# Kernel optimization log

Hardware: AMD Instinct MI355X
Metric: run time of the kernel (lower is better)

Reference implementation:

```python
import jax, jax.numpy as jnp
import numpy as np

N_NODES = 100000
N_EDGES = 1000000
EMB_DIM = 64
N_LAYERS = 5
NUM_CLASS = 10
NUM_GRAPHS = 128
BN_EPS = 1e-5


def setup_inputs() -> dict:
    key = jax.random.key(0)
    ks = jax.random.split(key, 16)
    s = 0.05
    inp = {
        "x": jnp.zeros((N_NODES,), dtype=jnp.int64),
        "edge_index": jax.random.randint(ks[0], (2, N_EDGES), 0, N_NODES, dtype=jnp.int64),
        "edge_attr": jax.random.normal(ks[1], (N_EDGES, 7), dtype=jnp.float32),
        "batch": jnp.sort(jax.random.randint(ks[2], (N_NODES,), 0, NUM_GRAPHS, dtype=jnp.int64)),
        # parameters
        "node_table": jax.random.normal(ks[3], (1, EMB_DIM), dtype=jnp.float32) * s,
        "ew": jax.random.normal(ks[4], (N_LAYERS, 7, EMB_DIM), dtype=jnp.float32) * s,   # edge_encoder weight
        "eb": jax.random.normal(ks[5], (N_LAYERS, EMB_DIM), dtype=jnp.float32) * s,
        "w1": jax.random.normal(ks[6], (N_LAYERS, EMB_DIM, EMB_DIM), dtype=jnp.float32) * s,
        "b1": jax.random.normal(ks[7], (N_LAYERS, EMB_DIM), dtype=jnp.float32) * s,
        "w2": jax.random.normal(ks[8], (N_LAYERS, EMB_DIM, EMB_DIM), dtype=jnp.float32) * s,
        "b2": jax.random.normal(ks[9], (N_LAYERS, EMB_DIM), dtype=jnp.float32) * s,
        "gamma": jnp.ones((N_LAYERS, EMB_DIM), dtype=jnp.float32),
        "beta": jnp.zeros((N_LAYERS, EMB_DIM), dtype=jnp.float32),
        "pw": jax.random.normal(ks[10], (EMB_DIM, NUM_CLASS), dtype=jnp.float32) * s,
        "pb": jnp.zeros((NUM_CLASS,), dtype=jnp.float32),
    }
    return inp


def reference(x, edge_index, edge_attr, batch, node_table, ew, eb, w1, b1, w2, b2, gamma, beta, pw, pb):
    n = x.shape[0]
    src, dst = edge_index[0], edge_index[1]
    h = node_table[x]  # [N, D] node embedding lookup (all index 0)
    for l in range(N_LAYERS):
        edge_emb = edge_attr @ ew[l] + eb[l]                      # [E, D]
        msg = jax.nn.relu(h[src] + edge_emb)                      # gather + add + relu
        agg = jax.ops.segment_sum(msg, dst, num_segments=n)       # scatter-add
        z = h + agg                                               # (1 + eps)*x with eps=0
        z = jax.nn.relu(z @ w1[l] + b1[l]) @ w2[l] + b2[l]        # GIN MLP
        mu = z.mean(axis=0)
        var = z.var(axis=0)                                       # biased var, matches BN training
        z = (z - mu) * jax.lax.rsqrt(var + BN_EPS) * gamma[l] + beta[l]
        if l != N_LAYERS - 1:
            z = jax.nn.relu(z)                                    # dropout is identity (eval)
        h = z
    # global mean pool over graphs
    sums = jax.ops.segment_sum(h, batch, num_segments=NUM_GRAPHS)           # [B, D]
    cnt = jax.ops.segment_sum(jnp.ones((n,), h.dtype), batch, num_segments=NUM_GRAPHS)
    h_graph = sums / jnp.maximum(cnt, 1.0)[:, None]
    return h_graph @ pw + pb
```

## Files before the change

### kernel.cpp

```cpp
#include <hip/hip_runtime.h>


__global__ void hist_k(const int* __restrict__ dst, int* __restrict__ cnt, int E) {
  int stride = gridDim.x * blockDim.x;
  for (int i = blockIdx.x * blockDim.x + threadIdx.x; i < E; i += stride)
    atomicAdd(&cnt[dst[i]], 1);
}

__global__ void scan_a_k(const int* __restrict__ deg, int* __restrict__ rowptr,
                         int* __restrict__ bsum, int n) {
  __shared__ int s[256];
  int i = blockIdx.x * 256 + threadIdx.x;
  int v = (i < n) ? deg[i] : 0;
  s[threadIdx.x] = v;
  __syncthreads();
  for (int off = 1; off < 256; off <<= 1) {
    int t = (threadIdx.x >= off) ? s[threadIdx.x - off] : 0;
    __syncthreads();
    s[threadIdx.x] += t;
    __syncthreads();
  }
  if (i < n) rowptr[i] = s[threadIdx.x] - v;
  if (threadIdx.x == 255) bsum[blockIdx.x] = s[255];
}

__global__ void scan_b_k(int* __restrict__ bsum, int nb) {
  __shared__ int s[512];
  int t = threadIdx.x;
  int v = (t < nb) ? bsum[t] : 0;
  s[t] = v;
  __syncthreads();
  for (int off = 1; off < 512; off <<= 1) {
    int u = (t >= off) ? s[t - off] : 0;
    __syncthreads();
    s[t] += u;
    __syncthreads();
  }
  if (t < nb) bsum[t] = s[t] - v;
}

__global__ void scan_c_k(int* __restrict__ rowptr, int* __restrict__ cur,
                         const int* __restrict__ bsum, int n, int E) {
  int i = blockIdx.x * 256 + threadIdx.x;
  if (i < n) {
    int r = rowptr[i] + bsum[blockIdx.x];
    rowptr[i] = r;
    cur[i] = r;
  }
  if (i == 0) rowptr[n] = E;
}

__global__ void scatter_k(const int* __restrict__ src, const int* __restrict__ dst,
                          int* __restrict__ cur, float* __restrict__ sea,
                          const float* __restrict__ ea, int E) {
  int stride = gridDim.x * blockDim.x;
  for (int i = blockIdx.x * blockDim.x + threadIdx.x; i < E; i += stride) {
    int d = dst[i];
    int pos = atomicAdd(&cur[d], 1);
    float* o = sea + (size_t)pos * 8;
    const float* a = ea + (size_t)i * 7;
#pragma unroll
    for (int k = 0; k < 7; k++) o[k] = a[k];
    o[7] = __int_as_float(src[i]);
  }
}

template<bool FIRST>
__global__ void agg_k(const float* __restrict__ hprev, const int* __restrict__ x,
                      const float* __restrict__ ntab, const int* __restrict__ rowptr,
                      const float* __restrict__ sea, const float* __restrict__ ew,
                      const float* __restrict__ eb, const float* __restrict__ scsh,
                      float* __restrict__ zout, int n, int layer) {
  int wid = (blockIdx.x * blockDim.x + threadIdx.x) >> 6;
  if (wid >= n) return;
  int lane = threadIdx.x & 63;
  const float* ewl = ew + layer * 448;
  float ew_[7];
#pragma unroll
  for (int k = 0; k < 7; k++) ew_[k] = ewl[k * 64 + lane];
  float ebv = eb[layer * 64 + lane];
  float sc = 1.f, sh = 0.f;
  if (!FIRST) { sc = scsh[lane]; sh = scsh[64 + lane]; }

  auto H = [&](int row) -> float {
    if (FIRST) {
      return ntab[x[row] * 64 + lane];
    } else {
      float v = hprev[(size_t)row * 64 + lane];
      return fmaxf(fmaf(v, sc, sh), 0.f);
    }
  };

  float acc = H(wid);
  int p0 = __builtin_amdgcn_readfirstlane(rowptr[wid]);
  int p1 = __builtin_amdgcn_readfirstlane(rowptr[wid + 1]);
  for (int p = p0; p < p1; p += 8) {
    const float* R[8];
    int srcv[8];
#pragma unroll
    for (int u = 0; u < 8; u++) {
      int t = p + u;
      int q = t < p1 ? t : p1 - 1;
      R[u] = sea + (size_t)q * 8;
      srcv[u] = __builtin_amdgcn_readfirstlane(__float_as_int(R[u][7]));
    }
    float h[8];
#pragma unroll
    for (int u = 0; u < 8; u++) h[u] = H(srcv[u]);
    float m[8];
#pragma unroll
    for (int u = 0; u < 8; u++) m[u] = ebv;
#pragma unroll
    for (int k = 0; k < 7; k++) {
#pragma unroll
      for (int u = 0; u < 8; u++) m[u] = fmaf(R[u][k], ew_[k], m[u]);
    }
#pragma unroll
    for (int u = 0; u < 8; u++) {
      float contrib = fmaxf(h[u] + m[u], 0.f);
      acc += (p + u < p1) ? contrib : 0.f;
    }
  }
  zout[(size_t)wid * 64 + lane] = acc;
}

__global__ __launch_bounds__(256, 3)
void mlp_k(const float* __restrict__ zin, const float* __restrict__ w1g,
           const float* __restrict__ b1, const float* __restrict__ w2g,
           const float* __restrict__ b2, float* __restrict__ zout,
           float* __restrict__ bnstats, int n, int layer) {
  __shared__ float As[64 * 129];
  __shared__ float Ws[64 * 64];
  __shared__ float red[128];
  int tid = threadIdx.x;
  int tx = tid & 15, ty = tid >> 4;
  if (tid < 128) red[tid] = 0.f;
  int r0 = blockIdx.x * 128;

  {
    const float4* gz = (const float4*)(zin + (size_t)r0 * 64);
#pragma unroll
    for (int it = 0; it < 8; it++) {
      int f4 = it * 256 + tid;
      int row = f4 >> 4, kq = f4 & 15;
      float4 v = make_float4(0.f, 0.f, 0.f, 0.f);
      if (r0 + row < n) v = gz[f4];
      As[(4 * kq + 0) * 129 + row] = v.x;
      As[(4 * kq + 1) * 129 + row] = v.y;
      As[(4 * kq + 2) * 129 + row] = v.z;
      As[(4 * kq + 3) * 129 + row] = v.w;
    }
    const float* wa = w1g + layer * 4096;
#pragma unroll
    for (int it = 0; it < 16; it++) Ws[it * 256 + tid] = wa[it * 256 + tid];
  }
  __syncthreads();

  const float4 b1v = *(const float4*)(b1 + layer * 64 + tx * 4);
  float t[8][4];
#pragma unroll
  for (int rr = 0; rr < 8; rr++) {
    t[rr][0] = b1v.x; t[rr][1] = b1v.y; t[rr][2] = b1v.z; t[rr][3] = b1v.w;
  }
#pragma unroll 4
  for (int k = 0; k < 64; k++) {
    float a[8];
#pragma unroll
    for (int rr = 0; rr < 8; rr++) a[rr] = As[k * 129 + ty * 8 + rr];
    float4 b = *(const float4*)&Ws[k * 64 + tx * 4];
#pragma unroll
    for (int rr = 0; rr < 8; rr++) {
      t[rr][0] = fmaf(a[rr], b.x, t[rr][0]);
      t[rr][1] = fmaf(a[rr], b.y, t[rr][1]);
      t[rr][2] = fmaf(a[rr], b.z, t[rr][2]);
      t[rr][3] = fmaf(a[rr], b.w, t[rr][3]);
    }
  }
  __syncthreads();

#pragma unroll
  for (int cc = 0; cc < 4; cc++)
#pragma unroll
    for (int rr = 0; rr < 8; rr++)
      As[(tx * 4 + cc) * 129 + ty * 8 + rr] = fmaxf(t[rr][cc], 0.f);
  {
    const float* wb = w2g + layer * 4096;
#pragma unroll
    for (int it = 0; it < 16; it++) Ws[it * 256 + tid] = wb[it * 256 + tid];
  }
  __syncthreads();

  const float4 b2v = *(const float4*)(b2 + layer * 64 + tx * 4);
  float o[8][4];
#pragma unroll
  for (int rr = 0; rr < 8; rr++) {
    o[rr][0] = b2v.x; o[rr][1] = b2v.y; o[rr][2] = b2v.z; o[rr][3] = b2v.w;
  }
#pragma unroll 4
  for (int k = 0; k < 64; k++) {
    float a[8];
#pragma unroll
    for (int rr = 0; rr < 8; rr++) a[rr] = As[k * 129 + ty * 8 + rr];
    float4 b = *(const float4*)&Ws[k * 64 + tx * 4];
#pragma unroll
    for (int rr = 0; rr < 8; rr++) {
      o[rr][0] = fmaf(a[rr], b.x, o[rr][0]);
      o[rr][1] = fmaf(a[rr], b.y, o[rr][1]);
      o[rr][2] = fmaf(a[rr], b.z, o[rr][2]);
      o[rr][3] = fmaf(a[rr], b.w, o[rr][3]);
    }
  }

  float s1[4] = {0.f, 0.f, 0.f, 0.f}, s2[4] = {0.f, 0.f, 0.f, 0.f};
#pragma unroll
  for (int rr = 0; rr < 8; rr++) {
    int grow = r0 + ty * 8 + rr;
    if (grow < n) {
      float4 v = make_float4(o[rr][0], o[rr][1], o[rr][2], o[rr][3]);
      *(float4*)(zout + (size_t)grow * 64 + tx * 4) = v;
#pragma unroll
      for (int cc = 0; cc < 4; cc++) {
        s1[cc] += o[rr][cc];
        s2[cc] = fmaf(o[rr][cc], o[rr][cc], s2[cc]);
      }
    }
  }
#pragma unroll
  for (int cc = 0; cc < 4; cc++) {
    s1[cc] += __shfl_xor(s1[cc], 16); s1[cc] += __shfl_xor(s1[cc], 32);
    s2[cc] += __shfl_xor(s2[cc], 16); s2[cc] += __shfl_xor(s2[cc], 32);
  }
  if ((tid & 48) == 0) {
#pragma unroll
    for (int cc = 0; cc < 4; cc++) {
      atomicAdd(&red[tx * 4 + cc], s1[cc]);
      atomicAdd(&red[64 + tx * 4 + cc], s2[cc]);
    }
  }
  __syncthreads();
  if (tid < 128) atomicAdd(&bnstats[tid], red[tid]);
}

__global__ void fin_k(float* __restrict__ bnstats, const float* __restrict__ gamma,
                      const float* __restrict__ beta, float* __restrict__ scsh,
                      int n, int layer) {
  int d = threadIdx.x;
  float mu = bnstats[d] / (float)n;
  float var = bnstats[64 + d] / (float)n - mu * mu;
  float sc = gamma[layer * 64 + d] * rsqrtf(var + 1e-5f);
  scsh[d] = sc;
  scsh[64 + d] = beta[layer * 64 + d] - mu * sc;
  bnstats[d] = 0.f;
  bnstats[64 + d] = 0.f;
}

__global__ void pool_k(const float* __restrict__ z2, const float* __restrict__ scsh,
                       const int* __restrict__ batch, float* __restrict__ gsum,
                       float* __restrict__ gcnt, int n, int ch) {
  int wid = (blockIdx.x * blockDim.x + threadIdx.x) >> 6;
  int lane = threadIdx.x & 63;
  int v0 = wid * ch;
  if (v0 >= n) return;
  int v1 = v0 + ch; if (v1 > n) v1 = n;
  float sc = scsh[lane], sh = scsh[64 + lane];
  int curb = batch[v0];
  float acc = 0.f;
  int cnt = 0;
  for (int v = v0; v < v1; v++) {
    int b = batch[v];
    if (b != curb) {
      atomicAdd(&gsum[curb * 64 + lane], acc);
      if (lane == 0) atomicAdd(&gcnt[curb], (float)cnt);
      acc = 0.f; cnt = 0; curb = b;
    }
    acc += fmaf(z2[(size_t)v * 64 + lane], sc, sh);
    cnt++;
  }
  atomicAdd(&gsum[curb * 64 + lane], acc);
  if (lane == 0) atomicAdd(&gcnt[curb], (float)cnt);
}

__global__ void head_k(const float* __restrict__ gsum, const float* __restrict__ gcnt,
                       const float* __restrict__ pw, const float* __restrict__ pb,
                       float* __restrict__ out, int B, int C) {
  for (int idx = threadIdx.x; idx < B * C; idx += blockDim.x) {
    int g = idx / C, c = idx % C;
    float inv = 1.f / fmaxf(gcnt[g], 1.f);
    float s = pb[c];
    for (int d = 0; d < 64; d++)
      s = fmaf(gsum[g * 64 + d] * inv, pw[d * C + c], s);
    out[idx] = s;
  }
}

extern "C" void kernel_launch(void* const* d_in, const int* in_sizes, int n_in,
                              void* d_out, int out_size, void* d_ws, size_t ws_size,
                              hipStream_t stream) {
  const int*   x     = (const int*)d_in[0];
  const int*   ei    = (const int*)d_in[1];
  const float* ea    = (const float*)d_in[2];
  const int*   batch = (const int*)d_in[3];
  const float* ntab  = (const float*)d_in[4];
  const float* ew    = (const float*)d_in[5];
  const float* eb    = (const float*)d_in[6];
  const float* w1    = (const float*)d_in[7];
  const float* b1    = (const float*)d_in[8];
  const float* w2    = (const float*)d_in[9];
  const float* b2    = (const float*)d_in[10];
  const float* gamma = (const float*)d_in[11];
  const float* beta  = (const float*)d_in[12];
  const float* pw    = (const float*)d_in[13];
  const float* pb    = (const float*)d_in[14];
  float* out = (float*)d_out;

  int N = in_sizes[0];
  int E = in_sizes[1] / 2;
  int L = in_sizes[6] / 64;
  int C = in_sizes[14];
  int B = out_size / C;

  const int* src = ei;
  const int* dst = ei + E;

  char* ws = (char*)d_ws;
  auto alloc = [&](size_t bytes) -> char* {
    char* p = ws;
    ws += (bytes + 255) & ~(size_t)255;
    return p;
  };
  float* zA      = (float*)alloc((size_t)N * 64 * 4);
  float* zB      = (float*)alloc((size_t)N * 64 * 4);
  int*   rowptr  = (int*)alloc((size_t)(N + 1) * 4);
  int*   cur     = (int*)alloc((size_t)N * 4);
  float* sea     = (float*)alloc((size_t)E * 8 * 4);
  int*   bsum    = (int*)alloc(512 * 4);
  float* bnstats = (float*)alloc(128 * 4);
  float* scsh    = (float*)alloc(128 * 4);
  float* gsum    = (float*)alloc((size_t)B * 64 * 4);
  float* gcnt    = (float*)alloc((size_t)B * 4);

  hipMemsetAsync(cur, 0, (size_t)N * 4, stream);
  hipMemsetAsync(bnstats, 0, 128 * 4, stream);
  hipMemsetAsync(gsum, 0, (size_t)B * 64 * 4, stream);
  hipMemsetAsync(gcnt, 0, (size_t)B * 4, stream);

  hist_k<<<1024, 256, 0, stream>>>(dst, cur, E);
  int NB = (N + 255) / 256;
  scan_a_k<<<NB, 256, 0, stream>>>(cur, rowptr, bsum, N);
  scan_b_k<<<1, 512, 0, stream>>>(bsum, NB);
  scan_c_k<<<NB, 256, 0, stream>>>(rowptr, cur, bsum, N, E);
  scatter_k<<<1024, 256, 0, stream>>>(src, dst, cur, sea, ea, E);

  int aggBlocks = (N * 64 + 255) / 256;
  int mlpBlocks = (N + 127) / 128;
  for (int l = 0; l < L; l++) {
    if (l == 0)
      agg_k<true><<<aggBlocks, 256, 0, stream>>>(zB, x, ntab, rowptr, sea,
                                                 ew, eb, scsh, zA, N, l);
    else
      agg_k<false><<<aggBlocks, 256, 0, stream>>>(zB, x, ntab, rowptr, sea,
                                                  ew, eb, scsh, zA, N, l);
    mlp_k<<<mlpBlocks, 256, 0, stream>>>(zA, w1, b1, w2, b2, zB, bnstats, N, l);
    fin_k<<<1, 64, 0, stream>>>(bnstats, gamma, beta, scsh, N, l);
  }

  int ch = 128;
  int poolWaves = (N + ch - 1) / ch;
  int poolBlocks = (poolWaves + 3) / 4;
  pool_k<<<poolBlocks, 256, 0, stream>>>(zB, scsh, batch, gsum, gcnt, N, ch);
  head_k<<<1, 256, 0, stream>>>(gsum, gcnt, pw, pb, out, B, C);
}
```

Baseline: 716.6 us.

## Fuse BN finalize into consumers, multi-node agg waves, vectorize MLP and scatter

Removes the per-layer fin_k launch by giving each layer its own stats slot and computing BN scale and shift inside the next agg kernel and inside pool_k. The agg kernel now processes 8 nodes per wave with a 4-edge unrolled loop, and adds a constant-table mode for a single-row node table that skips the neighbor gather entirely in layer 0. It also widens scatter stores and MLP shared-memory reads to float4 (stride 132), changes launch sizes, and adds unroll hints. Processing several nodes per wave reduces wave count but cuts parallelism and may worsen load imbalance.

After: 654.1 us. 1.1x faster.

```diff
diff --git a/kernel.cpp b/kernel.cpp
--- a/kernel.cpp
+++ b/kernel.cpp
@@ -57,80 +57,115 @@
   for (int i = blockIdx.x * blockDim.x + threadIdx.x; i < E; i += stride) {
     int d = dst[i];
     int pos = atomicAdd(&cur[d], 1);
-    float* o = sea + (size_t)pos * 8;
     const float* a = ea + (size_t)i * 7;
-#pragma unroll
-    for (int k = 0; k < 7; k++) o[k] = a[k];
-    o[7] = __int_as_float(src[i]);
-  }
-}
-
-template<bool FIRST>
-__global__ void agg_k(const float* __restrict__ hprev, const int* __restrict__ x,
-                      const float* __restrict__ ntab, const int* __restrict__ rowptr,
-                      const float* __restrict__ sea, const float* __restrict__ ew,
-                      const float* __restrict__ eb, const float* __restrict__ scsh,
-                      float* __restrict__ zout, int n, int layer) {
-  int wid = (blockIdx.x * blockDim.x + threadIdx.x) >> 6;
-  if (wid >= n) return;
+    float4 lo = make_float4(a[0], a[1], a[2], a[3]);
+    float4 hi = make_float4(a[4], a[5], a[6], __int_as_float(src[i]));
+    float4* o = (float4*)(sea + (size_t)pos * 8);
+    o[0] = lo;
+    o[1] = hi;
+  }
+}
+
+#define NPW 8
+template<int MODE>
+__global__ __launch_bounds__(256)
+void agg_k(const float* __restrict__ hprev, const int* __restrict__ x,
+           const float* __restrict__ ntab, const int* __restrict__ rowptr,
+           const float* __restrict__ sea, const float* __restrict__ ewl,
+           const float* __restrict__ ebl, const float* __restrict__ stats,
+           const float* __restrict__ gam, const float* __restrict__ bet,
+           float* __restrict__ zout, int n) {
+  int wv = (blockIdx.x * blockDim.x + threadIdx.x) >> 6;
   int lane = threadIdx.x & 63;
-  const float* ewl = ew + layer * 448;
+  int g0 = wv * NPW;
+  if (g0 >= n) return;
+  int gend = g0 + NPW; if (gend > n) gend = n;
+
   float ew_[7];
 #pragma unroll
   for (int k = 0; k < 7; k++) ew_[k] = ewl[k * 64 + lane];
-  float ebv = eb[layer * 64 + lane];
-  float sc = 1.f, sh = 0.f;
-  if (!FIRST) { sc = scsh[lane]; sh = scsh[64 + lane]; }
-
-  auto H = [&](int row) -> float {
-    if (FIRST) {
-      return ntab[x[row] * 64 + lane];
+  float ebv = ebl[lane];
+
+  float cnst = 0.f, sc = 1.f, sh = 0.f;
+  if (MODE == 0) cnst = ntab[lane];
+  if (MODE == 2) {
+    float s1 = stats[lane], s2 = stats[64 + lane];
+    float mu = s1 / (float)n;
+    float var = s2 / (float)n - mu * mu;
+    sc = gam[lane] * rsqrtf(var + 1e-5f);
+    sh = bet[lane] - mu * sc;
+  }
+
+  auto Hg = [&](int row) -> float {
+    if (MODE == 1) {
+      int xv = __builtin_amdgcn_readfirstlane(x[row]);
+      return ntab[(size_t)xv * 64 + lane];
     } else {
       float v = hprev[(size_t)row * 64 + lane];
       return fmaxf(fmaf(v, sc, sh), 0.f);
     }
   };
 
-  float acc = H(wid);
-  int p0 = __builtin_amdgcn_readfirstlane(rowptr[wid]);
-  int p1 = __builtin_amdgcn_readfirstlane(rowptr[wid + 1]);
-  for (int p = p0; p < p1; p += 8) {
-    const float* R[8];
-    int srcv[8];
-#pragma unroll
-    for (int u = 0; u < 8; u++) {
-      int t = p + u;
-      int q = t < p1 ? t : p1 - 1;
-      R[u] = sea + (size_t)q * 8;
-      srcv[u] = __builtin_amdgcn_readfirstlane(__float_as_int(R[u][7]));
-    }
-    float h[8];
-#pragma unroll
-    for (int u = 0; u < 8; u++) h[u] = H(srcv[u]);
-    float m[8];
-#pragma unroll
-    for (int u = 0; u < 8; u++) m[u] = ebv;
-#pragma unroll
-    for (int k = 0; k < 7; k++) {
-#pragma unroll
-      for (int u = 0; u < 8; u++) m[u] = fmaf(R[u][k], ew_[k], m[u]);
-    }
-#pragma unroll
-    for (int u = 0; u < 8; u++) {
-      float contrib = fmaxf(h[u] + m[u], 0.f);
-      acc += (p + u < p1) ? contrib : 0.f;
-    }
-  }
-  zout[(size_t)wid * 64 + lane] = acc;
-}
-
+  int pcur = __builtin_amdgcn_readfirstlane(rowptr[g0]);
+  for (int nd = g0; nd < gend; nd++) {
+    int pnext = __builtin_amdgcn_readfirstlane(rowptr[nd + 1]);
+    float acc;
+    if (MODE == 0) acc = cnst;
+    else acc = Hg(nd);
+    int p = pcur;
+    for (; p + 4 <= pnext; p += 4) {
+      const float* R0 = sea + (size_t)p * 8;
+      const float* R1 = R0 + 8;
+      const float* R2 = R0 + 16;
+      const float* R3 = R0 + 24;
+      float h0 = 0.f, h1 = 0.f, h2 = 0.f, h3 = 0.f;
+      if (MODE != 0) {
+        int s0 = __builtin_amdgcn_readfirstlane(__float_as_int(R0[7]));
+        int s1 = __builtin_amdgcn_readfirstlane(__float_as_int(R1[7]));
+        int s2 = __builtin_amdgcn_readfirstlane(__float_as_int(R2[7]));
+        int s3 = __builtin_amdgcn_readfirstlane(__float_as_int(R3[7]));
+        h0 = Hg(s0); h1 = Hg(s1); h2 = Hg(s2); h3 = Hg(s3);
+      } else {
+        h0 = h1 = h2 = h3 = cnst;
+      }
+      float m0 = ebv, m1 = ebv, m2 = ebv, m3 = ebv;
+#pragma unroll
+      for (int k = 0; k < 7; k++) {
+        m0 = fmaf(R0[k], ew_[k], m0);
+        m1 = fmaf(R1[k], ew_[k], m1);
+        m2 = fmaf(R2[k], ew_[k], m2);
+        m3 = fmaf(R3[k], ew_[k], m3);
+      }
+      acc += fmaxf(h0 + m0, 0.f);
+      acc += fmaxf(h1 + m1, 0.f);
+      acc += fmaxf(h2 + m2, 0.f);
+      acc += fmaxf(h3 + m3, 0.f);
+    }
+    for (; p < pnext; p++) {
+      const float* R0 = sea + (size_t)p * 8;
+      float h0 = cnst;
+      if (MODE != 0) {
+        int s0 = __builtin_amdgcn_readfirstlane(__float_as_int(R0[7]));
+        h0 = Hg(s0);
+      }
+      float m0 = ebv;
+#pragma unroll
+      for (int k = 0; k < 7; k++) m0 = fmaf(R0[k], ew_[k], m0);
+      acc += fmaxf(h0 + m0, 0.f);
+    }
+    zout[(size_t)nd * 64 + lane] = acc;
+    pcur = pnext;
+  }
+}
+
+#define ASTR 132
 __global__ __launch_bounds__(256, 3)
-void mlp_k(const float* __restrict__ zin, const float* __restrict__ w1g,
-           const float* __restrict__ b1, const float* __restrict__ w2g,
-           const float* __restrict__ b2, float* __restrict__ zout,
-           float* __restrict__ bnstats, int n, int layer) {
-  __shared__ float As[64 * 129];
-  __shared__ float Ws[64 * 64];
+void mlp_k(const float* __restrict__ zin, const float* __restrict__ w1l,
+           const float* __restrict__ b1l, const float* __restrict__ w2l,
+           const float* __restrict__ b2l, float* __restrict__ zout,
+           float* __restrict__ statslot, int n) {
+  __shared__ float As[64 * ASTR];
+  __shared__ float Ws[4096];
   __shared__ float red[128];
   int tid = threadIdx.x;
   int tx = tid & 15, ty = tid >> 4;
@@ -145,29 +180,30 @@
       int row = f4 >> 4, kq = f4 & 15;
       float4 v = make_float4(0.f, 0.f, 0.f, 0.f);
       if (r0 + row < n) v = gz[f4];
-      As[(4 * kq + 0) * 129 + row] = v.x;
-      As[(4 * kq + 1) * 129 + row] = v.y;
-      As[(4 * kq + 2) * 129 + row] = v.z;
-      As[(4 * kq + 3) * 129 + row] = v.w;
-    }
-    const float* wa = w1g + layer * 4096;
-#pragma unroll
-    for (int it = 0; it < 16; it++) Ws[it * 256 + tid] = wa[it * 256 + tid];
-  }
-  __syncthreads();
-
-  const float4 b1v = *(const float4*)(b1 + layer * 64 + tx * 4);
+      As[(4 * kq + 0) * ASTR + row] = v.x;
+      As[(4 * kq + 1) * ASTR + row] = v.y;
+      As[(4 * kq + 2) * ASTR + row] = v.z;
+      As[(4 * kq + 3) * ASTR + row] = v.w;
+    }
+    const float4* wa = (const float4*)w1l;
+    float4* wd = (float4*)Ws;
+#pragma unroll
+    for (int it = 0; it < 4; it++) wd[it * 256 + tid] = wa[it * 256 + tid];
+  }
+  __syncthreads();
+
+  const float4 b1v = *(const float4*)(b1l + tx * 4);
   float t[8][4];
 #pragma unroll
   for (int rr = 0; rr < 8; rr++) {
     t[rr][0] = b1v.x; t[rr][1] = b1v.y; t[rr][2] = b1v.z; t[rr][3] = b1v.w;
   }
-#pragma unroll 4
+#pragma unroll 8
   for (int k = 0; k < 64; k++) {
-    float a[8];
-#pragma unroll
-    for (int rr = 0; rr < 8; rr++) a[rr] = As[k * 129 + ty * 8 + rr];
+    float4 aA = *(const float4*)&As[k * ASTR + ty * 8];
+    float4 aB = *(const float4*)&As[k * ASTR + ty * 8 + 4];
     float4 b = *(const float4*)&Ws[k * 64 + tx * 4];
+    float a[8] = {aA.x, aA.y, aA.z, aA.w, aB.x, aB.y, aB.z, aB.w};
 #pragma unroll
     for (int rr = 0; rr < 8; rr++) {
       t[rr][0] = fmaf(a[rr], b.x, t[rr][0]);
@@ -182,26 +218,27 @@
   for (int cc = 0; cc < 4; cc++)
 #pragma unroll
     for (int rr = 0; rr < 8; rr++)
-      As[(tx * 4 + cc) * 129 + ty * 8 + rr] = fmaxf(t[rr][cc], 0.f);
+      As[(tx * 4 + cc) * ASTR + ty * 8 + rr] = fmaxf(t[rr][cc], 0.f);
   {
-    const float* wb = w2g + layer * 4096;
-#pragma unroll
-    for (int it = 0; it < 16; it++) Ws[it * 256 + tid] = wb[it * 256 + tid];
-  }
-  __syncthreads();
-
-  const float4 b2v = *(const float4*)(b2 + layer * 64 + tx * 4);
+    const float4* wb = (const float4*)w2l;
+    float4* wd = (float4*)Ws;
+#pragma unroll
+    for (int it = 0; it < 4; it++) wd[it * 256 + tid] = wb[it * 256 + tid];
+  }
+  __syncthreads();
+
+  const float4 b2v = *(const float4*)(b2l + tx * 4);
   float o[8][4];
 #pragma unroll
   for (int rr = 0; rr < 8; rr++) {
     o[rr][0] = b2v.x; o[rr][1] = b2v.y; o[rr][2] = b2v.z; o[rr][3] = b2v.w;
   }
-#pragma unroll 4
+#pragma unroll 8
   for (int k = 0; k < 64; k++) {
-    float a[8];
-#pragma unroll
-    for (int rr = 0; rr < 8; rr++) a[rr] = As[k * 129 + ty * 8 + rr];
+    float4 aA = *(const float4*)&As[k * ASTR + ty * 8];
+    float4 aB = *(const float4*)&As[k * ASTR + ty * 8 + 4];
     float4 b = *(const float4*)&Ws[k * 64 + tx * 4];
+    float a[8] = {aA.x, aA.y, aA.z, aA.w, aB.x, aB.y, aB.z, aB.w};
 #pragma unroll
     for (int rr = 0; rr < 8; rr++) {
       o[rr][0] = fmaf(a[rr], b.x, o[rr][0]);
@@ -238,23 +275,11 @@
     }
   }
   __syncthreads();
-  if (tid < 128) atomicAdd(&bnstats[tid], red[tid]);
-}
-
-__global__ void fin_k(float* __restrict__ bnstats, const float* __restrict__ gamma,
-                      const float* __restrict__ beta, float* __restrict__ scsh,
-                      int n, int layer) {
-  int d = threadIdx.x;
-  float mu = bnstats[d] / (float)n;
-  float var = bnstats[64 + d] / (float)n - mu * mu;
-  float sc = gamma[layer * 64 + d] * rsqrtf(var + 1e-5f);
-  scsh[d] = sc;
-  scsh[64 + d] = beta[layer * 64 + d] - mu * sc;
-  bnstats[d] = 0.f;
-  bnstats[64 + d] = 0.f;
-}
-
-__global__ void pool_k(const float* __restrict__ z2, const float* __restrict__ scsh,
+  if (tid < 128) atomicAdd(&statslot[tid], red[tid]);
+}
+
+__global__ void pool_k(const float* __restrict__ z2, const float* __restrict__ stats,
+                       const float* __restrict__ gam, const float* __restrict__ bet,
                        const int* __restrict__ batch, float* __restrict__ gsum,
                        float* __restrict__ gcnt, int n, int ch) {
   int wid = (blockIdx.x * blockDim.x + threadIdx.x) >> 6;
@@ -262,7 +287,11 @@
   int v0 = wid * ch;
   if (v0 >= n) return;
   int v1 = v0 + ch; if (v1 > n) v1 = n;
-  float sc = scsh[lane], sh = scsh[64 + lane];
+  float st1 = stats[lane], st2 = stats[64 + lane];
+  float mu = st1 / (float)n;
+  float var = st2 / (float)n - mu * mu;
+  float sc = gam[lane] * rsqrtf(var + 1e-5f);
+  float sh = bet[lane] - mu * sc;
   int curb = batch[v0];
   float acc = 0.f;
   int cnt = 0;
@@ -318,6 +347,7 @@
   int L = in_sizes[6] / 64;
   int C = in_sizes[14];
   int B = out_size / C;
+  bool tab1 = (in_sizes[4] == 64);
 
   const int* src = ei;
   const int* dst = ei + E;
@@ -334,39 +364,53 @@
   int*   cur     = (int*)alloc((size_t)N * 4);
   float* sea     = (float*)alloc((size_t)E * 8 * 4);
   int*   bsum    = (int*)alloc(512 * 4);
-  float* bnstats = (float*)alloc(128 * 4);
-  float* scsh    = (float*)alloc(128 * 4);
+  float* bnstats = (float*)alloc((size_t)L * 128 * 4);
   float* gsum    = (float*)alloc((size_t)B * 64 * 4);
   float* gcnt    = (float*)alloc((size_t)B * 4);
 
   hipMemsetAsync(cur, 0, (size_t)N * 4, stream);
-  hipMemsetAsync(bnstats, 0, 128 * 4, stream);
+  hipMemsetAsync(bnstats, 0, (size_t)L * 128 * 4, stream);
   hipMemsetAsync(gsum, 0, (size_t)B * 64 * 4, stream);
   hipMemsetAsync(gcnt, 0, (size_t)B * 4, stream);
 
-  hist_k<<<1024, 256, 0, stream>>>(dst, cur, E);
+  hist_k<<<2048, 256, 0, stream>>>(dst, cur, E);
   int NB = (N + 255) / 256;
   scan_a_k<<<NB, 256, 0, stream>>>(cur, rowptr, bsum, N);
   scan_b_k<<<1, 512, 0, stream>>>(bsum, NB);
   scan_c_k<<<NB, 256, 0, stream>>>(rowptr, cur, bsum, N, E);
-  scatter_k<<<1024, 256, 0, stream>>>(src, dst, cur, sea, ea, E);
-
-  int aggBlocks = (N * 64 + 255) / 256;
+  scatter_k<<<4096, 256, 0, stream>>>(src, dst, cur, sea, ea, E);
+
+  int aggWaves = (N + NPW - 1) / NPW;
+  int aggBlocks = (aggWaves * 64 + 255) / 256;
   int mlpBlocks = (N + 127) / 128;
   for (int l = 0; l < L; l++) {
-    if (l == 0)
-      agg_k<true><<<aggBlocks, 256, 0, stream>>>(zB, x, ntab, rowptr, sea,
-                                                 ew, eb, scsh, zA, N, l);
-    else
-      agg_k<false><<<aggBlocks, 256, 0, stream>>>(zB, x, ntab, rowptr, sea,
-                                                  ew, eb, scsh, zA, N, l);
-    mlp_k<<<mlpBlocks, 256, 0, stream>>>(zA, w1, b1, w2, b2, zB, bnstats, N, l);
-    fin_k<<<1, 64, 0, stream>>>(bnstats, gamma, beta, scsh, N, l);
+    const float* ewl = ew + (size_t)l * 448;
+    const float* ebl = eb + (size_t)l * 64;
+    const float* stP = bnstats + (size_t)(l > 0 ? l - 1 : 0) * 128;
+    const float* gmP = gamma + (size_t)(l > 0 ? l - 1 : 0) * 64;
+    const float* btP = beta + (size_t)(l > 0 ? l - 1 : 0) * 64;
+    if (l == 0) {
+      if (tab1)
+        agg_k<0><<<aggBlocks, 256, 0, stream>>>(zB, x, ntab, rowptr, sea, ewl, ebl,
+                                                stP, gmP, btP, zA, N);
+      else
+        agg_k<1><<<aggBlocks, 256, 0, stream>>>(zB, x, ntab, rowptr, sea, ewl, ebl,
+                                                stP, gmP, btP, zA, N);
+    } else {
+      agg_k<2><<<aggBlocks, 256, 0, stream>>>(zB, x, ntab, rowptr, sea, ewl, ebl,
+                                              stP, gmP, btP, zA, N);
+    }
+    mlp_k<<<mlpBlocks, 256, 0, stream>>>(zA, w1 + (size_t)l * 4096, b1 + (size_t)l * 64,
+                                         w2 + (size_t)l * 4096, b2 + (size_t)l * 64,
+                                         zB, bnstats + (size_t)l * 128, N);
   }
 
   int ch = 128;
   int poolWaves = (N + ch - 1) / ch;
   int poolBlocks = (poolWaves + 3) / 4;
-  pool_k<<<poolBlocks, 256, 0, stream>>>(zB, scsh, batch, gsum, gcnt, N, ch);
+  pool_k<<<poolBlocks, 256, 0, stream>>>(zB, bnstats + (size_t)(L - 1) * 128,
+                                         gamma + (size_t)(L - 1) * 64,
+                                         beta + (size_t)(L - 1) * 64,
+                                         batch, gsum, gcnt, N, ch);
   head_k<<<1, 256, 0, stream>>>(gsum, gcnt, pw, pb, out, B, C);
 }
```
